# Kernel optimization log

Measured on AMD Instinct MI355X. Metric: run time of the kernel, lower is better.

## Reference

```python
import jax, jax.numpy as jnp
import numpy as np

H = 128  # rnn_size

def setup_inputs() -> dict:
    key = jax.random.key(0)
    ks = jax.random.split(key, 12)
    B, T, F = 64, 2048, 64
    s = lambda k, shape, fan: jax.random.normal(k, shape, jnp.float32) * (1.0 / np.sqrt(fan))
    return {
        "x":  jax.random.normal(ks[0], (B, T, F), jnp.float32),
        # LSTM params (Keras gate order: i, f, c(g), o)
        "W":  s(ks[1], (F, 4 * H), F),
        "U":  s(ks[2], (H, 4 * H), H),
        "b":  jnp.zeros((4 * H,), jnp.float32),
        # Dense stack
        "W1": s(ks[3], (H, 128), H),   "b1": jnp.zeros((128,), jnp.float32),
        "W2": s(ks[4], (128, 128), 128), "b2": jnp.zeros((128,), jnp.float32),
        "W3": s(ks[5], (128, 32), 128),  "b3": jnp.zeros((32,), jnp.float32),
        "W4": s(ks[6], (32, 1), 32),     "b4": jnp.zeros((1,), jnp.float32),
    }

def _lstm(x, W, U, b):
    # x: [B,T,F] -> outputs h_t for all t: [B,T,H]
    B, T, _ = x.shape
    xp = jnp.einsum('btf,fg->btg', x, W) + b        # precompute input projection [B,T,4H]
    xp = jnp.transpose(xp, (1, 0, 2))               # [T,B,4H] for scan

    def step(carry, xt):
        h, c = carry
        z = xt + h @ U                              # [B,4H]
        i, f, g, o = jnp.split(z, 4, axis=-1)       # Keras gate order i,f,c,o
        i = jax.nn.sigmoid(i)
        f = jax.nn.sigmoid(f)
        g = jnp.tanh(g)
        o = jax.nn.sigmoid(o)
        c = f * c + i * g
        h = o * jnp.tanh(c)
        return (h, c), h

    h0 = jnp.zeros((B, H), x.dtype)
    c0 = jnp.zeros((B, H), x.dtype)
    _, hs = jax.lax.scan(step, (h0, c0), xp)        # hs: [T,B,H]
    return jnp.transpose(hs, (1, 0, 2))             # [B,T,H]

def reference(x, W, U, b, W1, b1, W2, b2, W3, b3, W4, b4):
    h = _lstm(x, W, U, b)                           # [B,T,H]
    h = h @ W1 + b1                                 # d1 (linear)
    h = jax.nn.relu(h @ W2 + b2)                    # d2
    h = jax.nn.relu(h @ W3 + b3)                    # d3
    out = jax.nn.sigmoid(h @ W4 + b4)               # d4 -> [B,T,1]
    return out.reshape(out.shape[0], -1, 1)         # Reshape((-1,1)) is identity here
```

## Files before the change

kernel.cpp:

```cpp
#include <hip/hip_runtime.h>
#include <hip/hip_fp16.h>
#include <cstdint>
#include <cstddef>

typedef _Float16 hh2   __attribute__((ext_vector_type(2)));
typedef _Float16 f16x8 __attribute__((ext_vector_type(8)));
typedef float    f32x4 __attribute__((ext_vector_type(4)));

__device__ __forceinline__ float fdot2u(unsigned a, unsigned b, float c) {
#if __has_builtin(__builtin_amdgcn_fdot2)
    return __builtin_amdgcn_fdot2(__builtin_bit_cast(hh2, a),
                                  __builtin_bit_cast(hh2, b), c, false);
#else
    float r;
    asm("v_dot2_f32_f16 %0, %1, %2, %3" : "=v"(r) : "v"(a), "v"(b), "v"(c));
    return r;
#endif
}

__device__ __forceinline__ unsigned packh2f(float x, float y) {
    hh2 v; v.x = (_Float16)x; v.y = (_Float16)y;
    return __builtin_bit_cast(unsigned, v);
}

__device__ __forceinline__ float ex2(float x) {
#if __has_builtin(__builtin_amdgcn_exp2f)
    return __builtin_amdgcn_exp2f(x);
#else
    return exp2f(x);
#endif
}
__device__ __forceinline__ float sig2(float x) {
    return __builtin_amdgcn_rcpf(1.f + ex2(x * -1.442695041f));
}
__device__ __forceinline__ float tanh2(float x) {
    return fmaf(2.f, __builtin_amdgcn_rcpf(1.f + ex2(x * -2.885390082f)), -1.f);
}
__device__ __forceinline__ float sigmoidf_fast(float x) {
    return __builtin_amdgcn_rcpf(1.f + __expf(-x));
}
__device__ __forceinline__ float tanhf_fast(float x) {
    float e = __expf(-2.f * fmaxf(x, -30.f));
    return (1.f - e) * __builtin_amdgcn_rcpf(1.f + e);
}

#define BAR_LGKM() asm volatile("s_waitcnt lgkmcnt(0)\n\ts_barrier" ::: "memory")

__global__ __launch_bounds__(512, 2)
void k_xprojT(const float* __restrict__ x, const float* __restrict__ W,
              const float* __restrict__ bias, __half* __restrict__ xpT,
              int B, int T)
{
    __shared__ unsigned short xst[2][16 * 64];

    const int tid = threadIdx.x;
    const int w   = tid >> 6;
    const int l   = tid & 63;
    const int lj  = l & 15;
    const int hi  = l >> 4;
    const int bb  = blockIdx.x >> 2;
    const int q   = blockIdx.x & 3;

    f16x8 Wf[4][2];
    float bc[4];
#pragma unroll
    for (int cg = 0; cg < 4; ++cg) {
        const int col = cg * 128 + w * 16 + lj;
#pragma unroll
        for (int kk = 0; kk < 2; ++kk)
#pragma unroll
            for (int j = 0; j < 8; ++j)
                Wf[cg][kk][j] = (_Float16)W[(size_t)(kk*32 + hi*8 + j) * 512 + col];
        bc[cg] = bias[col];
    }

    const int nch = (T / 4) / 16;
    const size_t rowbase = (size_t)bb * T + (size_t)q * (T / 4);

    const int srow = tid >> 5;
    const int scp  = tid & 31;

    float2 xn = *(const float2*)(x + (rowbase + srow) * 64 + scp * 2);

    for (int ch = 0; ch < nch; ++ch) {
        unsigned pk = packh2f(xn.x, xn.y);
        *(unsigned*)((char*)xst[ch & 1] +
            (((srow * 128 + scp * 4)) ^ ((srow & 7) << 4))) = pk;
        if (ch + 1 < nch)
            xn = *(const float2*)(x + (rowbase + (ch+1)*16 + srow) * 64 + scp * 2);
        BAR_LGKM();

        f16x8 Axf[2];
#pragma unroll
        for (int kk = 0; kk < 2; ++kk)
            Axf[kk] = *(const f16x8*)((char*)xst[ch & 1] +
                ((lj * 128 + kk * 64 + hi * 16) ^ ((lj & 7) << 4)));

        const size_t c8base = (rowbase + (size_t)ch * 16) >> 3;
#pragma unroll
        for (int cg = 0; cg < 4; ++cg) {
            f32x4 C = {bc[cg], bc[cg], bc[cg], bc[cg]};
            C = __builtin_amdgcn_mfma_f32_16x16x32_f16(Axf[0], Wf[cg][0], C, 0, 0, 0);
            C = __builtin_amdgcn_mfma_f32_16x16x32_f16(Axf[1], Wf[cg][1], C, 0, 0, 0);
            const int col = cg * 128 + w * 16 + lj;
            uint2 u;
            u.x = packh2f(C[0], C[1]);
            u.y = packh2f(C[2], C[3]);
            const size_t hidx = ((c8base + (hi >> 1)) * 512 + col) * 8 + (hi & 1) * 4;
            *(uint2*)((unsigned short*)xpT + hidx) = u;
        }
        BAR_LGKM();
    }
}

__global__ __launch_bounds__(512, 2)
void k_lstm5(const float* __restrict__ U, const __half* __restrict__ xpT,
             __half* __restrict__ hs, int T)
{
    __shared__ unsigned short hring[16][128];

    const int tid = threadIdx.x;
    const int w   = tid >> 6;
    const int l   = tid & 63;
    const int lj  = l & 15;
    const int hi  = l >> 4;
    const int bb  = blockIdx.x;

    f16x8 Bf[4][4];
#pragma unroll
    for (int g = 0; g < 4; ++g) {
        const int col = g * 128 + w * 16 + lj;
#pragma unroll
        for (int kk = 0; kk < 4; ++kk)
#pragma unroll
            for (int j = 0; j < 8; ++j)
                Bf[g][kk][j] = (_Float16)U[(size_t)(kk*32 + hi*8 + j) * 512 + col];
    }

    if (tid < 64) ((unsigned*)hring[15])[tid] = 0u;

    const uint4* __restrict__ xb = (const uint4*)xpT;
    const size_t xrow = (size_t)bb * (T / 8) * 512;
    int colg[4];
#pragma unroll
    for (int g = 0; g < 4; ++g) colg[g] = g * 128 + w * 16 + lj;

    uint4 qA[4], qB[4];
#pragma unroll
    for (int g = 0; g < 4; ++g) {
        qA[g] = xb[xrow + 0 * 512 + colg[g]];
        qB[g] = xb[xrow + 1 * 512 + colg[g]];
    }

    unsigned* __restrict__ hsw = (unsigned*)(hs + (size_t)bb * T * 128);
    float cst = 0.f;

    if (((w >> 2) ^ w) & 1) __builtin_amdgcn_s_setprio(1);

    f32x4 Cf[4] = {{0,0,0,0},{0,0,0,0},{0,0,0,0},{0,0,0,0}};

    BAR_LGKM();

    const int nbody = T / 16;
    for (int k = 0; k < nbody; ++k) {
#pragma unroll
        for (int p = 0; p < 16; ++p) {
            if (p == 2 && k > 0) {
                unsigned v = ((const unsigned*)hring[8])[tid];
                hsw[(size_t)(2*k - 1) * 512 + tid] = v;
            }
            if (p == 10) {
                unsigned v = ((const unsigned*)hring[0])[tid];
                hsw[(size_t)(2*k) * 512 + tid] = v;
            }
            if (p == 8) {
#pragma unroll
                for (int g = 0; g < 4; ++g)
                    qA[g] = xb[xrow + (size_t)(2*k + 2) * 512 + colg[g]];
            }

            const unsigned short* hrow = &hring[(p + 15) & 15][0];
            f16x8 Af[4];
#pragma unroll
            for (int kk = 0; kk < 4; ++kk)
                Af[kk] = *(const f16x8*)(hrow + kk * 32 + hi * 8);

#pragma unroll
            for (int g = 0; g < 4; ++g) {
                const uint4 qq = (p < 8) ? qA[g] : qB[g];
                const int wsel = (p & 7) >> 1;
                unsigned uw = (wsel == 0) ? qq.x : (wsel == 1) ? qq.y
                            : (wsel == 2) ? qq.z : qq.w;
                __half2 hh = __builtin_bit_cast(__half2, uw);
                Cf[g][0] = __half2float((p & 1) ? __high2half(hh) : __low2half(hh));
            }
#pragma unroll
            for (int kk = 0; kk < 4; ++kk)
#pragma unroll
                for (int g = 0; g < 4; ++g)
                    Cf[g] = __builtin_amdgcn_mfma_f32_16x16x32_f16(Af[kk], Bf[g][kk], Cf[g], 0, 0, 0);

            float iv = sig2(Cf[0][0]);
            float fv = sig2(Cf[1][0]);
            float gv = tanh2(Cf[2][0]);
            float ov = sig2(Cf[3][0]);
            cst = fmaf(fv, cst, iv * gv);
            float h = ov * tanh2(cst);

            if (l < 16)
                hring[p][w * 16 + lj] = __half_as_ushort(__float2half(h));

            if (p == 15) {
#pragma unroll
                for (int g = 0; g < 4; ++g)
                    qB[g] = xb[xrow + (size_t)(2*k + 3) * 512 + colg[g]];
            }
            BAR_LGKM();
        }
    }
    {
        unsigned v = ((const unsigned*)hring[8])[tid];
        hsw[(size_t)(T/8 - 1) * 512 + tid] = v;
    }
}

__global__ __launch_bounds__(512, 2)
void k_head(const __half* __restrict__ hs,
            const float* __restrict__ W1, const float* __restrict__ b1,
            const float* __restrict__ W2, const float* __restrict__ b2,
            const float* __restrict__ W3, const float* __restrict__ b3,
            const float* __restrict__ W4, const float* __restrict__ b4,
            float* __restrict__ out, int T)
{
    __shared__ unsigned short hstage[16 * 128];
    __shared__ unsigned short d1buf[16 * 128];
    __shared__ unsigned short d2buf[16 * 128];
    __shared__ unsigned short d3buf[16 * 40];

    const int tid = threadIdx.x;
    const int w   = tid >> 6;
    const int l   = tid & 63;
    const int lj  = l & 15;
    const int hi  = l >> 4;
    const int bb  = blockIdx.x >> 5;
    const int ch0 = (blockIdx.x & 31) * 4;

    const int col1 = w * 16 + lj;
    const int col3 = (w & 1) * 16 + lj;

    f16x8 W1f[4], W2f[4], W3f[4];
#pragma unroll
    for (int kk = 0; kk < 4; ++kk)
#pragma unroll
        for (int j = 0; j < 8; ++j) {
            W1f[kk][j] = (_Float16)W1[(size_t)(kk*32 + hi*8 + j) * 128 + col1];
            W2f[kk][j] = (_Float16)W2[(size_t)(kk*32 + hi*8 + j) * 128 + col1];
            W3f[kk][j] = (_Float16)W3[(size_t)(kk*32 + hi*8 + j) * 32 + col3];
        }
    const float b1c = b1[col1];
    const float b2c = b2[col1];
    const float b3c = b3[col3];
    unsigned w4p[16];
#pragma unroll
    for (int k2 = 0; k2 < 16; ++k2)
        w4p[k2] = packh2f(W4[2*k2], W4[2*k2 + 1]);
    const float b4v = b4[0];

    const __half* __restrict__ hsb = hs + (size_t)bb * T * 128;
    const int srow = tid >> 5;
    const int scp  = tid & 31;

    for (int ch = ch0; ch < ch0 + 4; ++ch) {
        const int t0 = ch * 16;
        uint2 hv = *(const uint2*)(hsb + (size_t)(t0 + srow) * 128 + scp * 4);
        *(uint2*)((char*)hstage + ((srow * 256 + scp * 8) ^ ((srow & 7) << 4))) = hv;
        __syncthreads();

        f16x8 A[4];
#pragma unroll
        for (int kk = 0; kk < 4; ++kk)
            A[kk] = *(const f16x8*)((char*)hstage +
                ((lj * 256 + kk * 64 + hi * 16) ^ ((lj & 7) << 4)));
        f32x4 C1 = {b1c, b1c, b1c, b1c};
#pragma unroll
        for (int kk = 0; kk < 4; ++kk)
            C1 = __builtin_amdgcn_mfma_f32_16x16x32_f16(A[kk], W1f[kk], C1, 0, 0, 0);
#pragma unroll
        for (int r = 0; r < 4; ++r) {
            const int row = hi * 4 + r;
            *(unsigned short*)((char*)d1buf + ((row * 256 + col1 * 2) ^ ((row & 7) << 4))) =
                __half_as_ushort(__float2half(C1[r]));
        }
        __syncthreads();

#pragma unroll
        for (int kk = 0; kk < 4; ++kk)
            A[kk] = *(const f16x8*)((char*)d1buf +
                ((lj * 256 + kk * 64 + hi * 16) ^ ((lj & 7) << 4)));
        f32x4 C2 = {b2c, b2c, b2c, b2c};
#pragma unroll
        for (int kk = 0; kk < 4; ++kk)
            C2 = __builtin_amdgcn_mfma_f32_16x16x32_f16(A[kk], W2f[kk], C2, 0, 0, 0);
#pragma unroll
        for (int r = 0; r < 4; ++r) {
            const int row = hi * 4 + r;
            *(unsigned short*)((char*)d2buf + ((row * 256 + col1 * 2) ^ ((row & 7) << 4))) =
                __half_as_ushort(__float2half(fmaxf(C2[r], 0.f)));
        }
        __syncthreads();

#pragma unroll
        for (int kk = 0; kk < 4; ++kk)
            A[kk] = *(const f16x8*)((char*)d2buf +
                ((lj * 256 + kk * 64 + hi * 16) ^ ((lj & 7) << 4)));
        f32x4 C3 = {b3c, b3c, b3c, b3c};
#pragma unroll
        for (int kk = 0; kk < 4; ++kk)
            C3 = __builtin_amdgcn_mfma_f32_16x16x32_f16(A[kk], W3f[kk], C3, 0, 0, 0);
        if (w < 2) {
#pragma unroll
            for (int r = 0; r < 4; ++r) {
                const int row = hi * 4 + r;
                d3buf[row * 40 + col3] =
                    __half_as_ushort(__float2half(fmaxf(C3[r], 0.f)));
            }
        }
        __syncthreads();

        if (w == 0 && l < 16) {
            const unsigned short* dr = &d3buf[l * 40];
            float s0 = b4v, s1 = 0.f;
#pragma unroll
            for (int qq = 0; qq < 4; ++qq) {
                uint4 v = *(const uint4*)(dr + qq * 8);
                s0 = fdot2u(v.x, w4p[qq*4 + 0], s0);
                s1 = fdot2u(v.y, w4p[qq*4 + 1], s1);
                s0 = fdot2u(v.z, w4p[qq*4 + 2], s0);
                s1 = fdot2u(v.w, w4p[qq*4 + 3], s1);
            }
            out[(size_t)bb * T + t0 + l] = sigmoidf_fast(s0 + s1);
        }
        __syncthreads();
    }
}

__global__ __launch_bounds__(512)
void k_lstm_fused(const float* __restrict__ U, const float* __restrict__ x,
                  const float* __restrict__ W, const float* __restrict__ bias,
                  __half* __restrict__ hs, int T)
{
    __shared__ __align__(16) unsigned hbuf[64];
    __shared__ float act[512];
    __shared__ __align__(16) unsigned xrow[32];

    const int g    = threadIdx.x;
    const int bb   = blockIdx.x;
    const int j    = g & 127;
    const int gate = g >> 7;

    unsigned ucol[64];
#pragma unroll
    for (int k2 = 0; k2 < 64; ++k2)
        ucol[k2] = packh2f(U[(2*k2)*512 + g], U[(2*k2+1)*512 + g]);
    unsigned wcol[32];
#pragma unroll
    for (int k2 = 0; k2 < 32; ++k2)
        wcol[k2] = packh2f(W[(2*k2)*512 + g], W[(2*k2+1)*512 + g]);
    const float bg = bias[g];
    const float2* __restrict__ xb2 = (const float2*)(x + (size_t)bb * T * 64);
    if (g < 32) { float2 x0 = xb2[g]; xrow[g] = packh2f(x0.x, x0.y); }
    if (g < 64) hbuf[g] = 0u;
    float c = 0.f;
    __half* __restrict__ hsb = hs + (size_t)bb * T * 128;
    __syncthreads();

    for (int t = 0; t < T; ++t) {
        float2 xn = make_float2(0.f, 0.f);
        if (g < 32 && t + 1 < T) xn = xb2[(size_t)(t + 1) * 32 + g];
        float a0 = bg, a1 = 0.f, a2 = 0.f, a3 = 0.f;
        const uint4* hr = (const uint4*)hbuf;
#pragma unroll
        for (int k8 = 0; k8 < 16; ++k8) {
            uint4 v = hr[k8];
            a0 = fdot2u(v.x, ucol[4*k8+0], a0);
            a1 = fdot2u(v.y, ucol[4*k8+1], a1);
            a2 = fdot2u(v.z, ucol[4*k8+2], a2);
            a3 = fdot2u(v.w, ucol[4*k8+3], a3);
        }
        const uint4* xr = (const uint4*)xrow;
#pragma unroll
        for (int k8 = 0; k8 < 8; ++k8) {
            uint4 v = xr[k8];
            a0 = fdot2u(v.x, wcol[4*k8+0], a0);
            a1 = fdot2u(v.y, wcol[4*k8+1], a1);
            a2 = fdot2u(v.z, wcol[4*k8+2], a2);
            a3 = fdot2u(v.w, wcol[4*k8+3], a3);
        }
        float z = (a0 + a1) + (a2 + a3);
        float a = (gate == 2) ? tanhf_fast(z) : sigmoidf_fast(z);
        act[g] = a;
        __syncthreads();
        float iv = act[j], fv = act[j + 128], gv = act[j + 256], ov = act[j + 384];
        c = fmaf(fv, c, iv * gv);
        float h = ov * tanhf_fast(c);
        if (gate == 0) {
            ((unsigned short*)hbuf)[j] = __half_as_ushort(__float2half(h));
            hsb[(size_t)t * 128 + j] = __float2half(h);
        }
        if (g < 32 && t + 1 < T) xrow[g] = packh2f(xn.x, xn.y);
        __syncthreads();
    }
}

template<bool RELU>
__global__ __launch_bounds__(512)
void k_fc128(const __half* __restrict__ in16, const float* __restrict__ Wg,
             const float* __restrict__ bias, __half* __restrict__ out16, int rows)
{
    __shared__ __align__(16) unsigned rowbuf[4 * 64];
    const int tid = threadIdx.x;
    const int n   = tid & 127;
    const int rs  = tid >> 7;
    unsigned wcol[64];
#pragma unroll
    for (int k2 = 0; k2 < 64; ++k2)
        wcol[k2] = packh2f(Wg[(2*k2)*128 + n], Wg[(2*k2+1)*128 + n]);
    const float bn = bias[n];
    for (int row0 = blockIdx.x * 4; row0 < rows; row0 += gridDim.x * 4) {
        if (tid < 256)
            rowbuf[tid] = ((const unsigned*)(in16 + (size_t)row0 * 128))[tid];
        __syncthreads();
        float a0 = bn, a1 = 0.f, a2 = 0.f, a3 = 0.f;
        const uint4* hr = (const uint4*)(rowbuf + rs * 64);
#pragma unroll
        for (int k8 = 0; k8 < 16; ++k8) {
            uint4 v = hr[k8];
            a0 = fdot2u(v.x, wcol[4*k8+0], a0);
            a1 = fdot2u(v.y, wcol[4*k8+1], a1);
            a2 = fdot2u(v.z, wcol[4*k8+2], a2);
            a3 = fdot2u(v.w, wcol[4*k8+3], a3);
        }
        float a = (a0 + a1) + (a2 + a3);
        if (RELU) a = fmaxf(a, 0.f);
        out16[(size_t)(row0 + rs) * 128 + n] = __float2half(a);
        __syncthreads();
    }
}

__global__ __launch_bounds__(512)
void k_l34(const __half* __restrict__ in16, const float* __restrict__ W3,
           const float* __restrict__ b3, const float* __restrict__ W4,
           const float* __restrict__ b4, float* __restrict__ out, int rows)
{
    __shared__ __align__(16) unsigned rowbuf[16 * 64];
    __shared__ __align__(16) unsigned short d3s[16 * 32];
    const int tid = threadIdx.x;
    const int n   = tid & 31;
    const int rs  = tid >> 5;
    unsigned w3col[64];
#pragma unroll
    for (int k2 = 0; k2 < 64; ++k2)
        w3col[k2] = packh2f(W3[(2*k2)*32 + n], W3[(2*k2+1)*32 + n]);
    unsigned w4p[16];
#pragma unroll
    for (int k2 = 0; k2 < 16; ++k2)
        w4p[k2] = packh2f(W4[2*k2], W4[2*k2+1]);
    const float b3n = b3[n], b4v = b4[0];
    for (int row0 = blockIdx.x * 16; row0 < rows; row0 += gridDim.x * 16) {
        rowbuf[tid]       = ((const unsigned*)(in16 + (size_t)row0 * 128))[tid];
        rowbuf[tid + 512] = ((const unsigned*)(in16 + (size_t)row0 * 128))[tid + 512];
        __syncthreads();
        float a0 = b3n, a1 = 0.f, a2 = 0.f, a3 = 0.f;
        const uint4* hr = (const uint4*)(rowbuf + rs * 64);
#pragma unroll
        for (int k8 = 0; k8 < 16; ++k8) {
            uint4 v = hr[k8];
            a0 = fdot2u(v.x, w3col[4*k8+0], a0);
            a1 = fdot2u(v.y, w3col[4*k8+1], a1);
            a2 = fdot2u(v.z, w3col[4*k8+2], a2);
            a3 = fdot2u(v.w, w3col[4*k8+3], a3);
        }
        float a = fmaxf((a0 + a1) + (a2 + a3), 0.f);
        d3s[rs * 32 + n] = __half_as_ushort(__float2half(a));
        __syncthreads();
        if (tid < 16) {
            const uint4* dp = (const uint4*)(d3s + tid * 32);
            float s0 = b4v, s1 = 0.f;
#pragma unroll
            for (int qq = 0; qq < 4; ++qq) {
                uint4 v = dp[qq];
                s0 = fdot2u(v.x, w4p[4*qq+0], s0);
                s1 = fdot2u(v.y, w4p[4*qq+1], s1);
                s0 = fdot2u(v.z, w4p[4*qq+2], s0);
                s1 = fdot2u(v.w, w4p[4*qq+3], s1);
            }
            out[row0 + tid] = sigmoidf_fast(s0 + s1);
        }
        __syncthreads();
    }
}

extern "C" void kernel_launch(void* const* d_in, const int* in_sizes, int n_in,
                              void* d_out, int out_size, void* d_ws, size_t ws_size,
                              hipStream_t stream)
{
    const float* x  = (const float*)d_in[0];
    const float* W  = (const float*)d_in[1];
    const float* U  = (const float*)d_in[2];
    const float* b  = (const float*)d_in[3];
    const float* W1 = (const float*)d_in[4];
    const float* b1 = (const float*)d_in[5];
    const float* W2 = (const float*)d_in[6];
    const float* b2 = (const float*)d_in[7];
    const float* W3 = (const float*)d_in[8];
    const float* b3 = (const float*)d_in[9];
    const float* W4 = (const float*)d_in[10];
    const float* b4 = (const float*)d_in[11];
    float* out = (float*)d_out;

    const int T    = 2048;
    const int rows = in_sizes[0] / 64;
    const int B    = rows / T;

    char* ws = (char*)d_ws;
    const size_t xp_bytes = (size_t)rows * 512 * sizeof(__half);
    const size_t hs_bytes = (size_t)rows * 128 * sizeof(__half);

    if (ws_size >= xp_bytes + hs_bytes) {
        __half* xpT  = (__half*)ws;
        __half* hs16 = (__half*)(ws + xp_bytes);
        k_xprojT<<<B * 4, 512, 0, stream>>>(x, W, b, xpT, B, T);
        k_lstm5<<<B, 512, 0, stream>>>(U, xpT, hs16, T);
        k_head<<<B * 32, 512, 0, stream>>>(hs16, W1, b1, W2, b2, W3, b3,
                                           W4, b4, out, T);
    } else {
        __half* hs16 = (__half*)ws;
        __half* d1   = (__half*)(ws + hs_bytes);
        __half* d2   = (__half*)ws;
        k_lstm_fused<<<B, 512, 0, stream>>>(U, x, W, b, hs16, T);
        k_fc128<false><<<1024, 512, 0, stream>>>(hs16, W1, b1, d1, rows);
        k_fc128<true ><<<1024, 512, 0, stream>>>(d1,  W2, b2, d2, rows);
        k_l34<<<1024, 512, 0, stream>>>(d2, W3, b3, W4, b4, out, rows);
    }
}
```

Baseline: 890.0 us.

## Stage LSTM input projections into LDS via async global-to-LDS loads

The recurrent LSTM kernel used to prefetch the precomputed input projections into registers (qA/qB) and pick the right half-word with selects at every step. It now uses global_load_lds to copy each 8-step chunk straight into a double-buffered LDS area, and each step reads its gate inputs back from LDS. The goal is lower register pressure and less per-step select/unpack work on the serial critical path. The cost is extra LDS reads and vmcnt waits at each chunk boundary. Each wave waits only on its own loads after the barrier, so another wave's data may not be guaranteed visible, which is a possible race.

```diff
diff --git a/kernel.cpp b/kernel.cpp
--- a/kernel.cpp
+++ b/kernel.cpp
@@ -45,6 +45,7 @@
 }
 
 #define BAR_LGKM() asm volatile("s_waitcnt lgkmcnt(0)\n\ts_barrier" ::: "memory")
+#define WAIT_VM0() asm volatile("s_waitcnt vmcnt(0)" ::: "memory")
 
 __global__ __launch_bounds__(512, 2)
 void k_xprojT(const float* __restrict__ x, const float* __restrict__ W,
@@ -114,10 +115,11 @@
 }
 
 __global__ __launch_bounds__(512, 2)
-void k_lstm5(const float* __restrict__ U, const __half* __restrict__ xpT,
+void k_lstm6(const float* __restrict__ U, const __half* __restrict__ xpT,
              __half* __restrict__ hs, int T)
 {
-    __shared__ unsigned short hring[16][128];
+    __shared__ __align__(16) unsigned short hring[16][128];
+    __shared__ __align__(16) unsigned short xstage[2][4096];
 
     const int tid = threadIdx.x;
     const int w   = tid >> 6;
@@ -139,18 +141,20 @@
 
     if (tid < 64) ((unsigned*)hring[15])[tid] = 0u;
 
-    const uint4* __restrict__ xb = (const uint4*)xpT;
-    const size_t xrow = (size_t)bb * (T / 8) * 512;
-    int colg[4];
-#pragma unroll
-    for (int g = 0; g < 4; ++g) colg[g] = g * 128 + w * 16 + lj;
-
-    uint4 qA[4], qB[4];
-#pragma unroll
-    for (int g = 0; g < 4; ++g) {
-        qA[g] = xb[xrow + 0 * 512 + colg[g]];
-        qB[g] = xb[xrow + 1 * 512 + colg[g]];
-    }
+    const char* __restrict__ xsrc = (const char*)xpT + (size_t)bb * (T / 8) * 8192;
+
+#define STAGE_XP(buf, c)                                                        \
+    __builtin_amdgcn_global_load_lds(                                           \
+        (const __attribute__((address_space(1))) unsigned*)(const void*)        \
+            (xsrc + (size_t)(c) * 8192 + w * 1024 + l * 16),                    \
+        (__attribute__((address_space(3))) unsigned*)(void*)                    \
+            ((char*)&xstage[buf][0] + w * 1024),                                \
+        16, 0, 0)
+
+    STAGE_XP(0, 0);
+    STAGE_XP(1, 1);
+
+    const int xcell = (w * 16 + lj) * 8;
 
     unsigned* __restrict__ hsw = (unsigned*)(hs + (size_t)bb * T * 128);
     float cst = 0.f;
@@ -159,12 +163,24 @@
 
     f32x4 Cf[4] = {{0,0,0,0},{0,0,0,0},{0,0,0,0},{0,0,0,0}};
 
-    BAR_LGKM();
+    WAIT_VM0();
+    __syncthreads();
 
     const int nbody = T / 16;
     for (int k = 0; k < nbody; ++k) {
 #pragma unroll
         for (int p = 0; p < 16; ++p) {
+            constexpr_helper:;
+            const int buf = (p >> 3) & 1;
+
+            if (p == 0) {
+                WAIT_VM0();
+                if (k > 0) STAGE_XP(1, 2 * k + 1);
+            }
+            if (p == 8) {
+                WAIT_VM0();
+                if (k + 1 < nbody) STAGE_XP(0, 2 * k + 2);
+            }
             if (p == 2 && k > 0) {
                 unsigned v = ((const unsigned*)hring[8])[tid];
                 hsw[(size_t)(2*k - 1) * 512 + tid] = v;
@@ -173,11 +189,6 @@
                 unsigned v = ((const unsigned*)hring[0])[tid];
                 hsw[(size_t)(2*k) * 512 + tid] = v;
             }
-            if (p == 8) {
-#pragma unroll
-                for (int g = 0; g < 4; ++g)
-                    qA[g] = xb[xrow + (size_t)(2*k + 2) * 512 + colg[g]];
-            }
 
             const unsigned short* hrow = &hring[(p + 15) & 15][0];
             f16x8 Af[4];
@@ -187,12 +198,8 @@
 
 #pragma unroll
             for (int g = 0; g < 4; ++g) {
-                const uint4 qq = (p < 8) ? qA[g] : qB[g];
-                const int wsel = (p & 7) >> 1;
-                unsigned uw = (wsel == 0) ? qq.x : (wsel == 1) ? qq.y
-                            : (wsel == 2) ? qq.z : qq.w;
-                __half2 hh = __builtin_bit_cast(__half2, uw);
-                Cf[g][0] = __half2float((p & 1) ? __high2half(hh) : __low2half(hh));
+                unsigned short xv = xstage[buf][g * 1024 + xcell + (p & 7)];
+                Cf[g][0] = __half2float(__ushort_as_half(xv));
             }
 #pragma unroll
             for (int kk = 0; kk < 4; ++kk)
@@ -210,11 +217,6 @@
             if (l < 16)
                 hring[p][w * 16 + lj] = __half_as_ushort(__float2half(h));
 
-            if (p == 15) {
-#pragma unroll
-                for (int g = 0; g < 4; ++g)
-                    qB[g] = xb[xrow + (size_t)(2*k + 3) * 512 + colg[g]];
-            }
             BAR_LGKM();
         }
     }
@@ -222,6 +224,7 @@
         unsigned v = ((const unsigned*)hring[8])[tid];
         hsw[(size_t)(T/8 - 1) * 512 + tid] = v;
     }
+#undef STAGE_XP
 }
 
 __global__ __launch_bounds__(512, 2)
@@ -530,7 +533,7 @@
         __half* xpT  = (__half*)ws;
         __half* hs16 = (__half*)(ws + xp_bytes);
         k_xprojT<<<B * 4, 512, 0, stream>>>(x, W, b, xpT, B, T);
-        k_lstm5<<<B, 512, 0, stream>>>(U, xpT, hs16, T);
+        k_lstm6<<<B, 512, 0, stream>>>(U, xpT, hs16, T);
         k_head<<<B * 32, 512, 0, stream>>>(hs16, W1, b1, W2, b2, W3, b3,
                                            W4, b4, out, T);
     } else {
```

New measurement: 959.6 us. +7.8%, slower.

## Quantize LSTM recurrent matmul to int8 MFMA with per-column scales

Applied to the files above, without the earlier changes.

The recurrent h@U product now uses int8 MFMA (16x16x64) instead of fp16 (16x16x32). U is quantized per gate column using an absmax scale, and h is quantized to int8 with a fixed scale of 127 in the shared ring buffer. This halves the MFMA count per step on the serial critical path. The hs output is now written directly per step from the lanes instead of as batched ring copies. The quantized hidden state adds error that compounds over 2048 recurrent steps and may exceed tolerance. The per-step global stores also add traffic inside the serial loop.

```diff
diff --git a/kernel.cpp b/kernel.cpp
--- a/kernel.cpp
+++ b/kernel.cpp
@@ -6,6 +6,7 @@
 typedef _Float16 hh2   __attribute__((ext_vector_type(2)));
 typedef _Float16 f16x8 __attribute__((ext_vector_type(8)));
 typedef float    f32x4 __attribute__((ext_vector_type(4)));
+typedef int      i32x4 __attribute__((ext_vector_type(4)));
 
 __device__ __forceinline__ float fdot2u(unsigned a, unsigned b, float c) {
 #if __has_builtin(__builtin_amdgcn_fdot2)
@@ -114,10 +115,10 @@
 }
 
 __global__ __launch_bounds__(512, 2)
-void k_lstm5(const float* __restrict__ U, const __half* __restrict__ xpT,
+void k_lstm7(const float* __restrict__ U, const __half* __restrict__ xpT,
              __half* __restrict__ hs, int T)
 {
-    __shared__ unsigned short hring[16][128];
+    __shared__ unsigned char hring[16][128];
 
     const int tid = threadIdx.x;
     const int w   = tid >> 6;
@@ -126,18 +127,35 @@
     const int hi  = l >> 4;
     const int bb  = blockIdx.x;
 
-    f16x8 Bf[4][4];
+    i32x4 Bq[4][2];
+    float dq[4];
 #pragma unroll
     for (int g = 0; g < 4; ++g) {
         const int col = g * 128 + w * 16 + lj;
-#pragma unroll
-        for (int kk = 0; kk < 4; ++kk)
-#pragma unroll
-            for (int j = 0; j < 8; ++j)
-                Bf[g][kk][j] = (_Float16)U[(size_t)(kk*32 + hi*8 + j) * 512 + col];
-    }
-
-    if (tid < 64) ((unsigned*)hring[15])[tid] = 0u;
+        float m = 0.f;
+        for (int k2 = 0; k2 < 128; ++k2)
+            m = fmaxf(m, fabsf(U[(size_t)k2 * 512 + col]));
+        const float s = (m > 0.f) ? 127.f / m : 0.f;
+        dq[g] = m * (1.f / (127.f * 127.f));
+#pragma unroll
+        for (int kk = 0; kk < 2; ++kk) {
+            int wds[4];
+#pragma unroll
+            for (int d = 0; d < 4; ++d) {
+                unsigned word = 0;
+#pragma unroll
+                for (int b = 0; b < 4; ++b) {
+                    int qv = (int)rintf(
+                        U[(size_t)(kk*64 + hi*16 + d*4 + b) * 512 + col] * s);
+                    word |= (unsigned)(qv & 255) << (8 * b);
+                }
+                wds[d] = (int)word;
+            }
+            Bq[g][kk] = (i32x4){wds[0], wds[1], wds[2], wds[3]};
+        }
+    }
+
+    if (tid < 32) ((unsigned*)hring[15])[tid] = 0u;
 
     const uint4* __restrict__ xb = (const uint4*)xpT;
     const size_t xrow = (size_t)bb * (T / 8) * 512;
@@ -152,39 +170,37 @@
         qB[g] = xb[xrow + 1 * 512 + colg[g]];
     }
 
-    unsigned* __restrict__ hsw = (unsigned*)(hs + (size_t)bb * T * 128);
+    __half* __restrict__ hsb = hs + (size_t)bb * T * 128;
     float cst = 0.f;
 
     if (((w >> 2) ^ w) & 1) __builtin_amdgcn_s_setprio(1);
 
-    f32x4 Cf[4] = {{0,0,0,0},{0,0,0,0},{0,0,0,0},{0,0,0,0}};
-
-    BAR_LGKM();
+    i32x4 Cq[4] = {{0,0,0,0},{0,0,0,0},{0,0,0,0},{0,0,0,0}};
+
+    __syncthreads();
 
     const int nbody = T / 16;
     for (int k = 0; k < nbody; ++k) {
 #pragma unroll
         for (int p = 0; p < 16; ++p) {
-            if (p == 2 && k > 0) {
-                unsigned v = ((const unsigned*)hring[8])[tid];
-                hsw[(size_t)(2*k - 1) * 512 + tid] = v;
-            }
-            if (p == 10) {
-                unsigned v = ((const unsigned*)hring[0])[tid];
-                hsw[(size_t)(2*k) * 512 + tid] = v;
-            }
             if (p == 8) {
 #pragma unroll
                 for (int g = 0; g < 4; ++g)
                     qA[g] = xb[xrow + (size_t)(2*k + 2) * 512 + colg[g]];
             }
 
-            const unsigned short* hrow = &hring[(p + 15) & 15][0];
-            f16x8 Af[4];
-#pragma unroll
-            for (int kk = 0; kk < 4; ++kk)
-                Af[kk] = *(const f16x8*)(hrow + kk * 32 + hi * 8);
-
+            const unsigned char* hrow = &hring[(p + 15) & 15][0];
+            i32x4 Aq0 = *(const i32x4*)(hrow + hi * 16);
+            i32x4 Aq1 = *(const i32x4*)(hrow + 64 + hi * 16);
+
+            Cq[0][0] = 0; Cq[1][0] = 0; Cq[2][0] = 0; Cq[3][0] = 0;
+#pragma unroll
+            for (int g = 0; g < 4; ++g) {
+                Cq[g] = __builtin_amdgcn_mfma_i32_16x16x64_i8(Aq0, Bq[g][0], Cq[g], 0, 0, 0);
+                Cq[g] = __builtin_amdgcn_mfma_i32_16x16x64_i8(Aq1, Bq[g][1], Cq[g], 0, 0, 0);
+            }
+
+            float zf[4];
 #pragma unroll
             for (int g = 0; g < 4; ++g) {
                 const uint4 qq = (p < 8) ? qA[g] : qB[g];
@@ -192,23 +208,22 @@
                 unsigned uw = (wsel == 0) ? qq.x : (wsel == 1) ? qq.y
                             : (wsel == 2) ? qq.z : qq.w;
                 __half2 hh = __builtin_bit_cast(__half2, uw);
-                Cf[g][0] = __half2float((p & 1) ? __high2half(hh) : __low2half(hh));
-            }
-#pragma unroll
-            for (int kk = 0; kk < 4; ++kk)
-#pragma unroll
-                for (int g = 0; g < 4; ++g)
-                    Cf[g] = __builtin_amdgcn_mfma_f32_16x16x32_f16(Af[kk], Bf[g][kk], Cf[g], 0, 0, 0);
-
-            float iv = sig2(Cf[0][0]);
-            float fv = sig2(Cf[1][0]);
-            float gv = tanh2(Cf[2][0]);
-            float ov = sig2(Cf[3][0]);
+                float xpf = __half2float((p & 1) ? __high2half(hh) : __low2half(hh));
+                zf[g] = fmaf((float)Cq[g][0], dq[g], xpf);
+            }
+
+            float iv = sig2(zf[0]);
+            float fv = sig2(zf[1]);
+            float gv = tanh2(zf[2]);
+            float ov = sig2(zf[3]);
             cst = fmaf(fv, cst, iv * gv);
             float h = ov * tanh2(cst);
 
-            if (l < 16)
-                hring[p][w * 16 + lj] = __half_as_ushort(__float2half(h));
+            if (l < 16) {
+                hsb[(size_t)(k * 16 + p) * 128 + w * 16 + lj] = __float2half(h);
+                hring[p][w * 16 + lj] =
+                    (unsigned char)(int)rintf(h * 127.f);
+            }
 
             if (p == 15) {
 #pragma unroll
@@ -217,10 +232,6 @@
             }
             BAR_LGKM();
         }
-    }
-    {
-        unsigned v = ((const unsigned*)hring[8])[tid];
-        hsw[(size_t)(T/8 - 1) * 512 + tid] = v;
     }
 }
 
@@ -530,7 +541,7 @@
         __half* xpT  = (__half*)ws;
         __half* hs16 = (__half*)(ws + xp_bytes);
         k_xprojT<<<B * 4, 512, 0, stream>>>(x, W, b, xpT, B, T);
-        k_lstm5<<<B, 512, 0, stream>>>(U, xpT, hs16, T);
+        k_lstm7<<<B, 512, 0, stream>>>(U, xpT, hs16, T);
         k_head<<<B * 32, 512, 0, stream>>>(hs16, W1, b1, W2, b2, W3, b3,
                                            W4, b4, out, T);
     } else {
```

After: 880.1 us. No clear change (-1.1%).
